# Performance work log

Measured on AMD Instinct MI355X. Metric: run time of the kernel, lower is better.

Reference implementation:

```python
import jax, jax.numpy as jnp
import numpy as np

D_MODEL = 1024
H = 16
D_K = D_MODEL // H
D_FF = 4096
EPS = 1e-6
NEG = -1e9


def layer_norm(x, alpha, beta):
    # Custom LN: scalar alpha/beta, unbiased std, eps added to std (not var)
    mean = jnp.mean(x, axis=-1, keepdims=True)
    std = jnp.std(x, axis=-1, ddof=1, keepdims=True)
    return alpha * (x - mean) / (std + EPS) + beta


def setup_inputs() -> dict:
    key = jax.random.key(0)
    ks = jax.random.split(key, 16)
    B, S = 4, 2048
    s = 1.0 / np.sqrt(D_MODEL)
    inp = {
        "x": jax.random.normal(ks[0], (B, S, D_MODEL), dtype=jnp.float32),
        "src_mask": jax.random.randint(ks[1], (B, 1, 1, S), 0, 2, dtype=jnp.int32),
        "wq": jax.random.normal(ks[2], (D_MODEL, D_MODEL), jnp.float32) * s,
        "bq": jnp.zeros((D_MODEL,), jnp.float32),
        "wk": jax.random.normal(ks[3], (D_MODEL, D_MODEL), jnp.float32) * s,
        "bk": jnp.zeros((D_MODEL,), jnp.float32),
        "wv": jax.random.normal(ks[4], (D_MODEL, D_MODEL), jnp.float32) * s,
        "bv": jnp.zeros((D_MODEL,), jnp.float32),
        "wo": jax.random.normal(ks[5], (D_MODEL, D_MODEL), jnp.float32) * s,
        "bo": jnp.zeros((D_MODEL,), jnp.float32),
        "w1": jax.random.normal(ks[6], (D_MODEL, D_FF), jnp.float32) * s,
        "b1": jnp.zeros((D_FF,), jnp.float32),
        "w2": jax.random.normal(ks[7], (D_FF, D_MODEL), jnp.float32) * (1.0 / np.sqrt(D_FF)),
        "b2": jnp.zeros((D_MODEL,), jnp.float32),
        "a1": jnp.ones((1,), jnp.float32),
        "be1": jnp.zeros((1,), jnp.float32),
        "a2": jnp.ones((1,), jnp.float32),
        "be2": jnp.zeros((1,), jnp.float32),
    }
    return inp


def reference(x, src_mask, wq, bq, wk, bk, wv, bv, wo, bo, w1, b1, w2, b2, a1, be1, a2, be2):
    B, S, _ = x.shape

    # --- residual 1: self-attention on pre-LN input (dropout = identity, eval) ---
    xn = layer_norm(x, a1, be1)
    q = (xn @ wq + bq).reshape(B, S, H, D_K).transpose(0, 2, 1, 3)  # [B,H,S,Dk]
    k = (xn @ wk + bk).reshape(B, S, H, D_K).transpose(0, 2, 1, 3)
    v = (xn @ wv + bv).reshape(B, S, H, D_K).transpose(0, 2, 1, 3)

    scores = jnp.einsum("bhqd,bhkd->bhqk", q, k) / jnp.sqrt(jnp.float32(D_K))
    scores = jnp.where(src_mask == 0, jnp.float32(NEG), scores)
    attn = jax.nn.softmax(scores, axis=-1)
    ctx = jnp.einsum("bhqk,bhkd->bhqd", attn, v)  # [B,H,S,Dk]
    ctx = ctx.transpose(0, 2, 1, 3).reshape(B, S, D_MODEL)
    attn_out = ctx @ wo + bo
    x = x + attn_out

    # --- residual 2: feed-forward on pre-LN input ---
    xn2 = layer_norm(x, a2, be2)
    ff = jax.nn.relu(xn2 @ w1 + b1) @ w2 + b2
    return x + ff
```

## Files before the change

### kernel.cpp

```cpp
#include <hip/hip_runtime.h>
#include <stdint.h>

typedef unsigned short u16;
typedef __attribute__((ext_vector_type(8))) short short8;
typedef __attribute__((ext_vector_type(4))) float f32x4;
typedef __attribute__((ext_vector_type(4))) u16 u16x4;
typedef __attribute__((ext_vector_type(4))) uint32_t u32x4;

#define NB 4
#define SEQ 2048
#define DM 1024
#define NH 16
#define DKh 64
#define DFF 4096
#define LOG2E 1.44269504089f

__device__ __forceinline__ u16 f2bf(float f) {
  union { float f; uint32_t u; } v; v.f = f;
  uint32_t u = v.u;
  return (u16)((u + 0x7FFFu + ((u >> 16) & 1u)) >> 16);
}

__device__ __forceinline__ uint32_t cvtpk(float lo, float hi) {
  uint32_t r;
  asm("v_cvt_pk_bf16_f32 %0, %1, %2" : "=v"(r) : "v"(lo), "v"(hi));
  return r;
}

__device__ __forceinline__ float fexp2(float x) {
  float r;
  asm("v_exp_f32 %0, %1" : "=v"(r) : "v"(x));
  return r;
}

__device__ __forceinline__ void gl16(const u16* g, u16* l) {
  __builtin_amdgcn_global_load_lds((const __attribute__((address_space(1))) void*)g,
                                   (__attribute__((address_space(3))) void*)l, 16, 0, 0);
}

__global__ __launch_bounds__(256) void transpose4_bf16(const float* __restrict__ s0,
                                                       const float* __restrict__ s1,
                                                       const float* __restrict__ s2,
                                                       const float* __restrict__ s3,
                                                       u16* __restrict__ d0,
                                                       u16* __restrict__ d1,
                                                       u16* __restrict__ d2,
                                                       u16* __restrict__ d3) {
  __shared__ float tile[32][33];
  int z = blockIdx.z;
  const float* src = (z == 0) ? s0 : (z == 1) ? s1 : (z == 2) ? s2 : s3;
  u16* dst = (z == 0) ? d0 : (z == 1) ? d1 : (z == 2) ? d2 : d3;
  int tx = threadIdx.x, ty = threadIdx.y;
  int c0 = blockIdx.x * 32, r0 = blockIdx.y * 32;
#pragma unroll
  for (int i = 0; i < 32; i += 8)
    tile[ty + i][tx] = src[(size_t)(r0 + ty + i) * DM + c0 + tx];
  __syncthreads();
#pragma unroll
  for (int i = 0; i < 32; i += 8)
    dst[(size_t)(c0 + ty + i) * DM + r0 + tx] = f2bf(tile[tx][ty + i]);
}

__global__ __launch_bounds__(256) void transpose_bf16(const float* __restrict__ src,
                                                      u16* __restrict__ dst, int R, int C) {
  __shared__ float tile[32][33];
  int tx = threadIdx.x, ty = threadIdx.y;
  int c0 = blockIdx.x * 32, r0 = blockIdx.y * 32;
#pragma unroll
  for (int i = 0; i < 32; i += 8)
    tile[ty + i][tx] = src[(size_t)(r0 + ty + i) * C + c0 + tx];
  __syncthreads();
#pragma unroll
  for (int i = 0; i < 32; i += 8)
    dst[(size_t)(c0 + ty + i) * R + r0 + tx] = f2bf(tile[tx][ty + i]);
}

__global__ __launch_bounds__(256) void bias_cat(const float* __restrict__ bq,
                                                const float* __restrict__ bk,
                                                const float* __restrict__ bv,
                                                float* __restrict__ o) {
  int i = blockIdx.x * 256 + threadIdx.x;
  if (i < 3072) o[i] = (i < 1024) ? bq[i] : ((i < 2048) ? bk[i - 1024] : bv[i - 2048]);
}

__global__ __launch_bounds__(1024) void compact_idx(const int* __restrict__ msk,
                                                    int* __restrict__ pinv,
                                                    int* __restrict__ lArr,
                                                    int* __restrict__ lpArr,
                                                    float* __restrict__ fbbc) {
  int b = blockIdx.x;
  int t = threadIdx.x;
  int lane = t & 63, w = t >> 6;
  int i0 = t * 2, i1 = t * 2 + 1;
  int m0 = msk[b * SEQ + i0] ? 1 : 0;
  int m1 = msk[b * SEQ + i1] ? 1 : 0;
  int s = m0 + m1;
  int run = s;
#pragma unroll
  for (int d = 1; d < 64; d <<= 1) {
    int v = __shfl_up(run, d);
    if (lane >= d) run += v;
  }
  __shared__ int wtot[16];
  __shared__ int woff[17];
  if (lane == 63) wtot[w] = run;
  __syncthreads();
  if (t == 0) {
    int acc = 0;
#pragma unroll
    for (int i = 0; i < 16; ++i) { woff[i] = acc; acc += wtot[i]; }
    woff[16] = acc;
  }
  __syncthreads();
  int excl = run - s + woff[w];
  pinv[b * SEQ + i0] = m0 ? excl : -1;
  pinv[b * SEQ + i1] = m1 ? (excl + m0) : -1;
  int L = woff[16];
  if (t == 0) {
    lArr[b] = L;
    int LP = (L + 63) & ~63;
    if (LP == 0) LP = 64;
    lpArr[b] = LP;
  }
  for (int l = t; l < SEQ; l += 1024)
    fbbc[b * SEQ + l] = (l < L) ? 0.0f : -1e9f;
}

__global__ __launch_bounds__(256) void ln_bf16(const float* __restrict__ x,
                                               u16* __restrict__ out,
                                               const float* __restrict__ alpha,
                                               const float* __restrict__ beta) {
  int row = blockIdx.x;
  const float4* xr = (const float4*)(x + (size_t)row * DM);
  int t = threadIdx.x;
  float4 v = xr[t];
  float s = v.x + v.y + v.z + v.w;
  float s2 = v.x * v.x + v.y * v.y + v.z * v.z + v.w * v.w;
#pragma unroll
  for (int m = 1; m < 64; m <<= 1) { s += __shfl_xor(s, m); s2 += __shfl_xor(s2, m); }
  __shared__ float red[8];
  int wid = t >> 6, lane = t & 63;
  if (lane == 0) { red[wid] = s; red[wid + 4] = s2; }
  __syncthreads();
  float S = red[0] + red[1] + red[2] + red[3];
  float S2 = red[4] + red[5] + red[6] + red[7];
  float mean = S * (1.0f / DM);
  float var = fmaxf((S2 - S * mean) * (1.0f / (DM - 1)), 0.0f);
  float inv = alpha[0] / (sqrtf(var) + 1e-6f);
  float bet = beta[0];
  u16x4 o;
  o[0] = f2bf((v.x - mean) * inv + bet);
  o[1] = f2bf((v.y - mean) * inv + bet);
  o[2] = f2bf((v.z - mean) * inv + bet);
  o[3] = f2bf((v.w - mean) * inv + bet);
  *(u16x4*)(out + (size_t)row * DM + t * 4) = o;
}

template <int MODE>
__global__ __launch_bounds__(512, 4) void gemm_v2(const u16* __restrict__ A,
                                                  const u16* __restrict__ WT,
                                                  const float* __restrict__ bias,
                                                  const float* __restrict__ resid,
                                                  void* __restrict__ outp,
                                                  const int* __restrict__ pinv,
                                                  int M, int N, int K, float qscale) {
  extern __shared__ u16 lds[];
  int tid = threadIdx.x;
  int lane = tid & 63, wid = tid >> 6;
  int lr = lane & 15, lg = lane >> 4;
  int wr = wid >> 1, wc = wid & 1;
  int nbx = N >> 7;
  int nwg = (M >> 8) * nbx;
  int lid = blockIdx.x;
  int swz = (lid & 7) * (nwg >> 3) + (lid >> 3);
  int m0 = (swz / nbx) << 8, n0 = (swz % nbx) << 7;

  int sr = tid >> 2;
  int sch = tid & 3;
  int scs = sch ^ ((sr >> 1) & 3);
  size_t a_src = (size_t)(m0 + sr) * K + scs * 8;
  size_t b_src = (size_t)(n0 + sr) * K + scs * 8;
  u16* a_dst = lds + sr * 32 + sch * 8;
  u16* b_dst = lds + 8192 + sr * 32 + sch * 8;

#define STAGE(B_, T_) do { \
    gl16(A + a_src + (size_t)(T_) * 32, a_dst + (B_) * 12288); \
    gl16(A + a_src + (size_t)128 * K + (size_t)(T_) * 32, a_dst + (B_) * 12288 + 4096); \
    gl16(WT + b_src + (size_t)(T_) * 32, b_dst + (B_) * 12288); \
  } while (0)

  int rchunk = (lg ^ ((lr >> 1) & 3)) * 8;
  int offA[4], offB[4];
#pragma unroll
  for (int i = 0; i < 4; ++i) offA[i] = (wr * 64 + i * 16 + lr) * 32 + rchunk;
#pragma unroll
  for (int j = 0; j < 4; ++j) offB[j] = 8192 + (wc * 64 + j * 16 + lr) * 32 + rchunk;

  f32x4 acc[4][4] = {};

  int NT = K >> 5;
  STAGE(0, 0);
  STAGE(1, 1);
  asm volatile("s_waitcnt vmcnt(3)" ::: "memory");
  __builtin_amdgcn_s_barrier();

  int buf = 0;
  for (int t = 0; t < NT; ++t) {
    const u16* la = lds + buf * 12288;
    int b2 = buf - 1; if (b2 < 0) b2 += 3;
    short8 af[4], bfr[4];
#pragma unroll
    for (int i = 0; i < 4; ++i) af[i] = *(const short8*)&la[offA[i]];
#pragma unroll
    for (int j = 0; j < 4; ++j) bfr[j] = *(const short8*)&la[offB[j]];
    if (t + 2 < NT) STAGE(b2, t + 2);
    __builtin_amdgcn_s_setprio(1);
#pragma unroll
    for (int i = 0; i < 4; ++i)
#pragma unroll
      for (int j = 0; j < 4; ++j)
        acc[i][j] = __builtin_amdgcn_mfma_f32_16x16x32_bf16(af[i], bfr[j], acc[i][j], 0, 0, 0);
    __builtin_amdgcn_s_setprio(0);
    if (t < NT - 2) asm volatile("s_waitcnt vmcnt(3)" ::: "memory");
    else            asm volatile("s_waitcnt vmcnt(0)" ::: "memory");
    __builtin_amdgcn_s_barrier();
    __builtin_amdgcn_sched_barrier(0);
    buf = (buf == 2) ? 0 : buf + 1;
  }
#undef STAGE

#pragma unroll
  for (int i = 0; i < 4; ++i) {
#pragma unroll
    for (int j = 0; j < 4; ++j) {
      int col = n0 + wc * 64 + j * 16 + lr;
      float bi = bias[col];
      int rbase = m0 + wr * 64 + i * 16 + lg * 4;
      if (MODE == 2) {
        float* o = (float*)outp;
#pragma unroll
        for (int r = 0; r < 4; ++r) {
          size_t idx = (size_t)(rbase + r) * N + col;
          o[idx] = resid[idx] + acc[i][j][r] + bi;
        }
      } else if (MODE == 3) {
        u16* o = (u16*)outp;
#pragma unroll
        for (int r = 0; r < 4; ++r)
          o[(size_t)(rbase + r) * N + col] = f2bf(fmaxf(acc[i][j][r] + bi, 0.0f));
      } else {
        u16* qb = (u16*)outp;
        int which = col >> 10, nc = col & 1023;
        int hh = nc >> 6, dd = nc & 63;
        int bb = rbase >> 11, ss = rbase & 2047;
        if (which == 0) {
#pragma unroll
          for (int r = 0; r < 4; ++r)
            qb[((size_t)(bb * NH + hh) * SEQ + (ss + r)) * DKh + dd] = f2bf((acc[i][j][r] + bi) * qscale);
        } else {
          int4 p4 = *(const int4*)(pinv + bb * SEQ + ss);
          int pos[4] = {p4.x, p4.y, p4.z, p4.w};
          if (which == 1) {
            u16* kcb = qb + (size_t)(8u << 20);
#pragma unroll
            for (int r = 0; r < 4; ++r)
              if (pos[r] >= 0)
                kcb[((size_t)(bb * NH + hh) * SEQ + pos[r]) * DKh + dd] = f2bf(acc[i][j][r] + bi);
          } else {
            u16* vcb = qb + (size_t)2 * (8u << 20);
#pragma unroll
            for (int r = 0; r < 4; ++r)
              if (pos[r] >= 0) {
                int l = pos[r];
                int lo = l & 63;
                int pi = ((lo >> 4) & 1) * 32 + ((lo >> 2) & 3) * 8 + (lo >> 5) * 4 + (lo & 3);
                vcb[((size_t)(bb * NH + hh) * DKh + dd) * SEQ + (l & ~63) + pi] = f2bf(acc[i][j][r] + bi);
              }
          }
        }
      }
    }
  }
}

__global__ __launch_bounds__(512) void attn_fwd(const u16* __restrict__ q,
                                                const u16* __restrict__ kc,
                                                const u16* __restrict__ vc,
                                                const int* __restrict__ lArr,
                                                const int* __restrict__ lpArr,
                                                const float* __restrict__ fbbc,
                                                u16* __restrict__ ctx) {
  __shared__ u16 lds[2][16384];
  int tid = threadIdx.x;
  int wid = tid >> 6, lane = tid & 63;
  int lr = lane & 15, lg = lane >> 4;
  int bh = blockIdx.x;
  int b = bh >> 4, hh = bh & 15;
  int q0 = blockIdx.y * 256 + wid * 32;
  const u16* qbase = q + (size_t)bh * SEQ * DKh;
  const u16* kcb = kc + (size_t)bh * SEQ * DKh;
  const u16* vcb = vc + (size_t)bh * DKh * SEQ;
  const float* fbbase = fbbc + b * SEQ;
  int Lb = lArr[b];
  int LP = lpArr[b];

  short8 qf[2][2];
#pragma unroll
  for (int i = 0; i < 2; ++i)
#pragma unroll
    for (int kk = 0; kk < 2; ++kk)
      qf[i][kk] = *(const short8*)(qbase + (size_t)(q0 + i * 16 + lr) * DKh + kk * 32 + lg * 8);

  int srow = tid >> 3;
  int schk = tid & 7;
  int ks0 = srow * 64 + ((schk ^ (srow & 7)) * 8);
  int vs0 = srow * SEQ + ((schk ^ (srow & 7)) * 8);
  int dst0 = tid * 8;

#define STAGE(B_, KV0) do { \
    gl16(kcb + (size_t)(KV0) * 64 + ks0, &lds[B_][dst0]); \
    gl16(kcb + (size_t)((KV0) + 64) * 64 + ks0, &lds[B_][dst0 + 4096]); \
    gl16(vcb + (size_t)(KV0) + vs0, &lds[B_][dst0 + 8192]); \
    gl16(vcb + (size_t)(KV0) + 64 + vs0, &lds[B_][dst0 + 12288]); \
  } while (0)

  int swzc = (lr & 7) << 3;

  f32x4 ot[2][4] = {};
  float mrow[2] = {-3e38f, -3e38f};
  float lsum[2] = {0.0f, 0.0f};

  STAGE(0, 0);
  asm volatile("s_waitcnt vmcnt(0)" ::: "memory");
  __builtin_amdgcn_s_barrier();

  int buf = 0;
  for (int kv0 = 0; kv0 < LP; kv0 += 128) {
    bool more = (kv0 + 128 < LP);
    if (more) STAGE(buf ^ 1, kv0 + 128);
    if (more) asm volatile("s_waitcnt vmcnt(4)" ::: "memory");
    else      asm volatile("s_waitcnt vmcnt(0)" ::: "memory");
    __builtin_amdgcn_s_barrier();

#pragma unroll
    for (int sB = 0; sB < 2; ++sB) {
      const u16* Ks = &lds[buf][sB * 4096];
      const u16* Vs = &lds[buf][8192 + sB * 4096];
      int kvs = kv0 + sB * 64;

      f32x4 st[2][4] = {};
      __builtin_amdgcn_s_setprio(1);
#pragma unroll
      for (int kk = 0; kk < 2; ++kk) {
        short8 kf[4];
#pragma unroll
        for (int j = 0; j < 4; ++j)
          kf[j] = *(const short8*)&Ks[(j * 16 + lr) * 64 + ((kk * 32 + lg * 8) ^ swzc)];
#pragma unroll
        for (int i = 0; i < 2; ++i)
#pragma unroll
          for (int j = 0; j < 4; ++j)
            st[i][j] = __builtin_amdgcn_mfma_f32_16x16x32_bf16(kf[j], qf[i][kk], st[i][j], 0, 0, 0);
      }
      __builtin_amdgcn_s_setprio(0);

      bool tail = (kvs + 64 > Lb);

      u32x4 pa[2][2];
#pragma unroll
      for (int i = 0; i < 2; ++i) {
        float p[4][4];
        if (tail) {
#pragma unroll
          for (int j = 0; j < 4; ++j) {
            float4 f4 = *(const float4*)(fbbase + kvs + j * 16 + lg * 4);
            p[j][0] = st[i][j][0] + f4.x;
            p[j][1] = st[i][j][1] + f4.y;
            p[j][2] = st[i][j][2] + f4.z;
            p[j][3] = st[i][j][3] + f4.w;
          }
        } else {
#pragma unroll
          for (int j = 0; j < 4; ++j)
#pragma unroll
            for (int r = 0; r < 4; ++r) p[j][r] = st[i][j][r];
        }
        float mx = -3e38f;
#pragma unroll
        for (int j = 0; j < 4; ++j)
#pragma unroll
          for (int r = 0; r < 4; ++r) mx = fmaxf(mx, p[j][r]);
        mx = fmaxf(mx, __shfl_xor(mx, 16));
        mx = fmaxf(mx, __shfl_xor(mx, 32));
        float mnew = fmaxf(mrow[i], mx);
        if (!__all(mnew - mrow[i] <= 8.0f)) {
          float corr = fexp2(mrow[i] - mnew);
          lsum[i] *= corr;
#pragma unroll
          for (int jd = 0; jd < 4; ++jd)
#pragma unroll
            for (int r = 0; r < 4; ++r) ot[i][jd][r] *= corr;
          mrow[i] = mnew;
        }
        float ps = 0.0f;
#pragma unroll
        for (int j = 0; j < 4; ++j)
#pragma unroll
          for (int r = 0; r < 4; ++r) {
            float pv = fexp2(p[j][r] - mrow[i]);
            p[j][r] = pv;
            ps += pv;
          }
        ps += __shfl_xor(ps, 16);
        ps += __shfl_xor(ps, 32);
        lsum[i] += ps;
#pragma unroll
        for (int ks = 0; ks < 2; ++ks) {
          pa[i][ks][0] = cvtpk(p[ks][0], p[ks][1]);
          pa[i][ks][1] = cvtpk(p[ks][2], p[ks][3]);
          pa[i][ks][2] = cvtpk(p[ks + 2][0], p[ks + 2][1]);
          pa[i][ks][3] = cvtpk(p[ks + 2][2], p[ks + 2][3]);
        }
      }

      __builtin_amdgcn_s_setprio(1);
#pragma unroll
      for (int ks = 0; ks < 2; ++ks) {
        short8 vf[4];
#pragma unroll
        for (int jd = 0; jd < 4; ++jd)
          vf[jd] = *(const short8*)&Vs[(jd * 16 + lr) * 64 + ((ks * 32 + lg * 8) ^ swzc)];
#pragma unroll
        for (int i = 0; i < 2; ++i)
#pragma unroll
          for (int jd = 0; jd < 4; ++jd)
            ot[i][jd] = __builtin_amdgcn_mfma_f32_16x16x32_bf16(vf[jd], *(short8*)&pa[i][ks], ot[i][jd], 0, 0, 0);
      }
      __builtin_amdgcn_s_setprio(0);
    }
    __builtin_amdgcn_s_barrier();
    buf ^= 1;
  }
#undef STAGE

  asm volatile("s_waitcnt vmcnt(0)" ::: "memory");
  __builtin_amdgcn_s_barrier();

  float inv0 = 1.0f / lsum[0], inv1 = 1.0f / lsum[1];
  u16* ep = &lds[0][wid * 2048];
#pragma unroll
  for (int i = 0; i < 2; ++i) {
    float inv = i ? inv1 : inv0;
#pragma unroll
    for (int jd = 0; jd < 4; ++jd) {
      uint32_t w0 = cvtpk(ot[i][jd][0] * inv, ot[i][jd][1] * inv);
      uint32_t w1 = cvtpk(ot[i][jd][2] * inv, ot[i][jd][3] * inv);
      uint32_t pk2[2] = {w0, w1};
      *(u16x4*)&ep[(i * 16 + lr) * 64 + ((jd * 16 + lg * 4) ^ swzc)] = *(u16x4*)pk2;
    }
  }
  __syncthreads();
  int q_ = lane >> 1;
  size_t orow = ((size_t)b * SEQ + q0 + q_) * DM + hh * DKh;
#pragma unroll
  for (int it = 0; it < 4; ++it) {
    int dc = (lane & 1) * 32 + it * 8;
    short8 vv = *(const short8*)&ep[q_ * 64 + (dc ^ ((q_ & 7) << 3))];
    *(short8*)(ctx + orow + dc) = vv;
  }
}

extern "C" void kernel_launch(void* const* d_in, const int* in_sizes, int n_in,
                              void* d_out, int out_size, void* d_ws, size_t ws_size,
                              hipStream_t stream) {
  const float* x   = (const float*)d_in[0];
  const int*   msk = (const int*)d_in[1];
  const float* wq  = (const float*)d_in[2];
  const float* bq  = (const float*)d_in[3];
  const float* wk  = (const float*)d_in[4];
  const float* bk  = (const float*)d_in[5];
  const float* wv  = (const float*)d_in[6];
  const float* bv  = (const float*)d_in[7];
  const float* wo  = (const float*)d_in[8];
  const float* bo  = (const float*)d_in[9];
  const float* w1  = (const float*)d_in[10];
  const float* b1  = (const float*)d_in[11];
  const float* w2  = (const float*)d_in[12];
  const float* b2  = (const float*)d_in[13];
  const float* a1  = (const float*)d_in[14];
  const float* be1 = (const float*)d_in[15];
  const float* a2  = (const float*)d_in[16];
  const float* be2 = (const float*)d_in[17];
  float* out = (float*)d_out;

  u16* wqT = (u16*)d_ws;
  u16* wkT = wqT + (1u << 20);
  u16* wvT = wkT + (1u << 20);
  u16* woT = wvT + (1u << 20);
  u16* w1T = woT + (1u << 20);
  u16* w2T = w1T + (4u << 20);
  u16* xn  = w2T + (4u << 20);
  u16* qb  = xn  + (8u << 20);
  u16* kb  = qb  + (8u << 20);
  u16* vtb = kb  + (8u << 20);
  u16* ctx = vtb + (8u << 20);
  u16* hb  = qb;
  float* bcat = (float*)ctx;
  int*   pinv = (int*)(ctx + (8u << 20));
  int*   lArr = pinv + NB * SEQ;
  int*   lpArr = lArr + 16;
  float* fbbc = (float*)(lpArr + 16);

  (void)hipFuncSetAttribute((const void*)gemm_v2<0>, hipFuncAttributeMaxDynamicSharedMemorySize, 72 * 1024);
  (void)hipFuncSetAttribute((const void*)gemm_v2<2>, hipFuncAttributeMaxDynamicSharedMemorySize, 72 * 1024);
  (void)hipFuncSetAttribute((const void*)gemm_v2<3>, hipFuncAttributeMaxDynamicSharedMemorySize, 72 * 1024);

  dim3 tb(32, 8);
  transpose4_bf16<<<dim3(32, 32, 4), tb, 0, stream>>>(wq, wk, wv, wo, wqT, wkT, wvT, woT);
  transpose_bf16<<<dim3(128, 32), tb, 0, stream>>>(w1, w1T, DM, DFF);
  transpose_bf16<<<dim3(32, 128), tb, 0, stream>>>(w2, w2T, DFF, DM);
  bias_cat<<<12, 256, 0, stream>>>(bq, bk, bv, bcat);
  compact_idx<<<NB, 1024, 0, stream>>>(msk, pinv, lArr, lpArr, fbbc);

  ln_bf16<<<NB * SEQ, 256, 0, stream>>>(x, xn, a1, be1);

  gemm_v2<0><<<768, 512, 72 * 1024, stream>>>(xn, wqT, bcat, nullptr, qb, pinv, NB * SEQ, 3 * DM, DM, 0.125f * LOG2E);

  attn_fwd<<<dim3(NB * NH, SEQ / 256), 512, 0, stream>>>(qb, kb, vtb, lArr, lpArr, fbbc, ctx);

  gemm_v2<2><<<256, 512, 72 * 1024, stream>>>(ctx, woT, bo, x, out, nullptr, NB * SEQ, DM, DM, 1.0f);

  ln_bf16<<<NB * SEQ, 256, 0, stream>>>(out, xn, a2, be2);

  gemm_v2<3><<<1024, 512, 72 * 1024, stream>>>(xn, w1T, b1, nullptr, hb, nullptr, NB * SEQ, DFF, DM, 1.0f);

  gemm_v2<2><<<256, 512, 72 * 1024, stream>>>(hb, w2T, b2, out, out, nullptr, NB * SEQ, DM, DFF, 1.0f);
}
```

Measured before the change: 349.3 us.

## Double GEMM K-tile to 64 with 8-chunk XOR swizzle and merge prep kernels

The GEMM now stages a 64-wide K slice per pipeline step instead of 32. It uses six 16-byte global-to-LDS loads per thread and a new 8-way XOR swizzle, and issues two MFMA k-substeps per barrier. This halves the number of loop iterations and barriers per GEMM. In exchange, LDS use doubles to 144 KB for three buffers and launch bounds drop to 2 blocks per SM, which reduces occupancy. The separate weight-transpose and bias-concat kernels are also merged into one prep launch to cut launch overhead.

```diff
diff --git a/kernel.cpp b/kernel.cpp
--- a/kernel.cpp
+++ b/kernel.cpp
@@ -38,34 +38,34 @@
                                    (__attribute__((address_space(3))) void*)l, 16, 0, 0);
 }
 
-__global__ __launch_bounds__(256) void transpose4_bf16(const float* __restrict__ s0,
-                                                       const float* __restrict__ s1,
-                                                       const float* __restrict__ s2,
-                                                       const float* __restrict__ s3,
-                                                       u16* __restrict__ d0,
-                                                       u16* __restrict__ d1,
-                                                       u16* __restrict__ d2,
-                                                       u16* __restrict__ d3) {
+__global__ __launch_bounds__(256) void prep(const float* __restrict__ wq, const float* __restrict__ wk,
+                                            const float* __restrict__ wv, const float* __restrict__ wo,
+                                            const float* __restrict__ w1, const float* __restrict__ w2,
+                                            u16* __restrict__ wqT, u16* __restrict__ wkT,
+                                            u16* __restrict__ wvT, u16* __restrict__ woT,
+                                            u16* __restrict__ w1T, u16* __restrict__ w2T,
+                                            const float* __restrict__ bq, const float* __restrict__ bk,
+                                            const float* __restrict__ bv, float* __restrict__ bcat) {
+  int idx = blockIdx.x;
+  int tx = threadIdx.x, ty = threadIdx.y;
+  if (idx >= 12288) {
+    int i = (idx - 12288) * 256 + ty * 32 + tx;
+    if (i < 3072) bcat[i] = (i < 1024) ? bq[i] : ((i < 2048) ? bk[i - 1024] : bv[i - 2048]);
+    return;
+  }
+  const float* src; u16* dst; int R, C, bx, by;
+  if (idx < 4096) {
+    int z = idx >> 10;
+    src = (z == 0) ? wq : (z == 1) ? wk : (z == 2) ? wv : wo;
+    dst = (z == 0) ? wqT : (z == 1) ? wkT : (z == 2) ? wvT : woT;
+    R = DM; C = DM; int i = idx & 1023; bx = i & 31; by = i >> 5;
+  } else if (idx < 8192) {
+    src = w1; dst = w1T; R = DM; C = DFF; int i = idx - 4096; bx = i & 127; by = i >> 7;
+  } else {
+    src = w2; dst = w2T; R = DFF; C = DM; int i = idx - 8192; bx = i & 31; by = i >> 5;
+  }
   __shared__ float tile[32][33];
-  int z = blockIdx.z;
-  const float* src = (z == 0) ? s0 : (z == 1) ? s1 : (z == 2) ? s2 : s3;
-  u16* dst = (z == 0) ? d0 : (z == 1) ? d1 : (z == 2) ? d2 : d3;
-  int tx = threadIdx.x, ty = threadIdx.y;
-  int c0 = blockIdx.x * 32, r0 = blockIdx.y * 32;
-#pragma unroll
-  for (int i = 0; i < 32; i += 8)
-    tile[ty + i][tx] = src[(size_t)(r0 + ty + i) * DM + c0 + tx];
-  __syncthreads();
-#pragma unroll
-  for (int i = 0; i < 32; i += 8)
-    dst[(size_t)(c0 + ty + i) * DM + r0 + tx] = f2bf(tile[tx][ty + i]);
-}
-
-__global__ __launch_bounds__(256) void transpose_bf16(const float* __restrict__ src,
-                                                      u16* __restrict__ dst, int R, int C) {
-  __shared__ float tile[32][33];
-  int tx = threadIdx.x, ty = threadIdx.y;
-  int c0 = blockIdx.x * 32, r0 = blockIdx.y * 32;
+  int c0 = bx * 32, r0 = by * 32;
 #pragma unroll
   for (int i = 0; i < 32; i += 8)
     tile[ty + i][tx] = src[(size_t)(r0 + ty + i) * C + c0 + tx];
@@ -73,14 +73,6 @@
 #pragma unroll
   for (int i = 0; i < 32; i += 8)
     dst[(size_t)(c0 + ty + i) * R + r0 + tx] = f2bf(tile[tx][ty + i]);
-}
-
-__global__ __launch_bounds__(256) void bias_cat(const float* __restrict__ bq,
-                                                const float* __restrict__ bk,
-                                                const float* __restrict__ bv,
-                                                float* __restrict__ o) {
-  int i = blockIdx.x * 256 + threadIdx.x;
-  if (i < 3072) o[i] = (i < 1024) ? bq[i] : ((i < 2048) ? bk[i - 1024] : bv[i - 2048]);
 }
 
 __global__ __launch_bounds__(1024) void compact_idx(const int* __restrict__ msk,
@@ -157,7 +149,7 @@
 }
 
 template <int MODE>
-__global__ __launch_bounds__(512, 4) void gemm_v2(const u16* __restrict__ A,
+__global__ __launch_bounds__(512, 2) void gemm_v2(const u16* __restrict__ A,
                                                   const u16* __restrict__ WT,
                                                   const float* __restrict__ bias,
                                                   const float* __restrict__ resid,
@@ -175,53 +167,66 @@
   int swz = (lid & 7) * (nwg >> 3) + (lid >> 3);
   int m0 = (swz / nbx) << 8, n0 = (swz % nbx) << 7;
 
-  int sr = tid >> 2;
-  int sch = tid & 3;
-  int scs = sch ^ ((sr >> 1) & 3);
-  size_t a_src = (size_t)(m0 + sr) * K + scs * 8;
-  size_t b_src = (size_t)(n0 + sr) * K + scs * 8;
-  u16* a_dst = lds + sr * 32 + sch * 8;
-  u16* b_dst = lds + 8192 + sr * 32 + sch * 8;
+  int sr2 = tid >> 3;
+  int sch2 = tid & 7;
+  int csrc8 = (sch2 ^ (sr2 & 7)) * 8;
+  size_t a_src = (size_t)(m0 + sr2) * K + csrc8;
+  size_t b_src = (size_t)(n0 + sr2) * K + csrc8;
+  u16* dstb = lds + tid * 8;
 
 #define STAGE(B_, T_) do { \
-    gl16(A + a_src + (size_t)(T_) * 32, a_dst + (B_) * 12288); \
-    gl16(A + a_src + (size_t)128 * K + (size_t)(T_) * 32, a_dst + (B_) * 12288 + 4096); \
-    gl16(WT + b_src + (size_t)(T_) * 32, b_dst + (B_) * 12288); \
+    const u16* as_ = A + a_src + (size_t)(T_) * 64; \
+    gl16(as_,                   dstb + (B_) * 24576); \
+    gl16(as_ + (size_t)64 * K,  dstb + (B_) * 24576 + 4096); \
+    gl16(as_ + (size_t)128 * K, dstb + (B_) * 24576 + 8192); \
+    gl16(as_ + (size_t)192 * K, dstb + (B_) * 24576 + 12288); \
+    const u16* bs_ = WT + b_src + (size_t)(T_) * 64; \
+    gl16(bs_,                   dstb + (B_) * 24576 + 16384); \
+    gl16(bs_ + (size_t)64 * K,  dstb + (B_) * 24576 + 20480); \
   } while (0)
 
-  int rchunk = (lg ^ ((lr >> 1) & 3)) * 8;
+  int xo8 = lr & 7;
+  int ckk[2] = {((0 + lg) ^ xo8) * 8, ((4 + lg) ^ xo8) * 8};
   int offA[4], offB[4];
 #pragma unroll
-  for (int i = 0; i < 4; ++i) offA[i] = (wr * 64 + i * 16 + lr) * 32 + rchunk;
-#pragma unroll
-  for (int j = 0; j < 4; ++j) offB[j] = 8192 + (wc * 64 + j * 16 + lr) * 32 + rchunk;
+  for (int i = 0; i < 4; ++i) offA[i] = (wr * 64 + i * 16 + lr) * 64;
+#pragma unroll
+  for (int j = 0; j < 4; ++j) offB[j] = 16384 + (wc * 64 + j * 16 + lr) * 64;
 
   f32x4 acc[4][4] = {};
 
-  int NT = K >> 5;
+  int NT = K >> 6;
   STAGE(0, 0);
   STAGE(1, 1);
-  asm volatile("s_waitcnt vmcnt(3)" ::: "memory");
+  asm volatile("s_waitcnt vmcnt(6)" ::: "memory");
   __builtin_amdgcn_s_barrier();
 
   int buf = 0;
   for (int t = 0; t < NT; ++t) {
-    const u16* la = lds + buf * 12288;
+    const u16* la = lds + buf * 24576;
     int b2 = buf - 1; if (b2 < 0) b2 += 3;
-    short8 af[4], bfr[4];
-#pragma unroll
-    for (int i = 0; i < 4; ++i) af[i] = *(const short8*)&la[offA[i]];
-#pragma unroll
-    for (int j = 0; j < 4; ++j) bfr[j] = *(const short8*)&la[offB[j]];
+    short8 af[4][2], bfr[4][2];
+#pragma unroll
+    for (int i = 0; i < 4; ++i) {
+      af[i][0] = *(const short8*)&la[offA[i] + ckk[0]];
+      af[i][1] = *(const short8*)&la[offA[i] + ckk[1]];
+    }
+#pragma unroll
+    for (int j = 0; j < 4; ++j) {
+      bfr[j][0] = *(const short8*)&la[offB[j] + ckk[0]];
+      bfr[j][1] = *(const short8*)&la[offB[j] + ckk[1]];
+    }
     if (t + 2 < NT) STAGE(b2, t + 2);
     __builtin_amdgcn_s_setprio(1);
 #pragma unroll
-    for (int i = 0; i < 4; ++i)
-#pragma unroll
-      for (int j = 0; j < 4; ++j)
-        acc[i][j] = __builtin_amdgcn_mfma_f32_16x16x32_bf16(af[i], bfr[j], acc[i][j], 0, 0, 0);
+    for (int kk = 0; kk < 2; ++kk)
+#pragma unroll
+      for (int i = 0; i < 4; ++i)
+#pragma unroll
+        for (int j = 0; j < 4; ++j)
+          acc[i][j] = __builtin_amdgcn_mfma_f32_16x16x32_bf16(af[i][kk], bfr[j][kk], acc[i][j], 0, 0, 0);
     __builtin_amdgcn_s_setprio(0);
-    if (t < NT - 2) asm volatile("s_waitcnt vmcnt(3)" ::: "memory");
+    if (t < NT - 2) asm volatile("s_waitcnt vmcnt(6)" ::: "memory");
     else            asm volatile("s_waitcnt vmcnt(0)" ::: "memory");
     __builtin_amdgcn_s_barrier();
     __builtin_amdgcn_sched_barrier(0);
@@ -511,28 +516,25 @@
   int*   lpArr = lArr + 16;
   float* fbbc = (float*)(lpArr + 16);
 
-  (void)hipFuncSetAttribute((const void*)gemm_v2<0>, hipFuncAttributeMaxDynamicSharedMemorySize, 72 * 1024);
-  (void)hipFuncSetAttribute((const void*)gemm_v2<2>, hipFuncAttributeMaxDynamicSharedMemorySize, 72 * 1024);
-  (void)hipFuncSetAttribute((const void*)gemm_v2<3>, hipFuncAttributeMaxDynamicSharedMemorySize, 72 * 1024);
+  (void)hipFuncSetAttribute((const void*)gemm_v2<0>, hipFuncAttributeMaxDynamicSharedMemorySize, 144 * 1024);
+  (void)hipFuncSetAttribute((const void*)gemm_v2<2>, hipFuncAttributeMaxDynamicSharedMemorySize, 144 * 1024);
+  (void)hipFuncSetAttribute((const void*)gemm_v2<3>, hipFuncAttributeMaxDynamicSharedMemorySize, 144 * 1024);
 
   dim3 tb(32, 8);
-  transpose4_bf16<<<dim3(32, 32, 4), tb, 0, stream>>>(wq, wk, wv, wo, wqT, wkT, wvT, woT);
-  transpose_bf16<<<dim3(128, 32), tb, 0, stream>>>(w1, w1T, DM, DFF);
-  transpose_bf16<<<dim3(32, 128), tb, 0, stream>>>(w2, w2T, DFF, DM);
-  bias_cat<<<12, 256, 0, stream>>>(bq, bk, bv, bcat);
+  prep<<<12300, tb, 0, stream>>>(wq, wk, wv, wo, w1, w2, wqT, wkT, wvT, woT, w1T, w2T, bq, bk, bv, bcat);
   compact_idx<<<NB, 1024, 0, stream>>>(msk, pinv, lArr, lpArr, fbbc);
 
   ln_bf16<<<NB * SEQ, 256, 0, stream>>>(x, xn, a1, be1);
 
-  gemm_v2<0><<<768, 512, 72 * 1024, stream>>>(xn, wqT, bcat, nullptr, qb, pinv, NB * SEQ, 3 * DM, DM, 0.125f * LOG2E);
+  gemm_v2<0><<<768, 512, 144 * 1024, stream>>>(xn, wqT, bcat, nullptr, qb, pinv, NB * SEQ, 3 * DM, DM, 0.125f * LOG2E);
 
   attn_fwd<<<dim3(NB * NH, SEQ / 256), 512, 0, stream>>>(qb, kb, vtb, lArr, lpArr, fbbc, ctx);
 
-  gemm_v2<2><<<256, 512, 72 * 1024, stream>>>(ctx, woT, bo, x, out, nullptr, NB * SEQ, DM, DM, 1.0f);
+  gemm_v2<2><<<256, 512, 144 * 1024, stream>>>(ctx, woT, bo, x, out, nullptr, NB * SEQ, DM, DM, 1.0f);
 
   ln_bf16<<<NB * SEQ, 256, 0, stream>>>(out, xn, a2, be2);
 
-  gemm_v2<3><<<1024, 512, 72 * 1024, stream>>>(xn, w1T, b1, nullptr, hb, nullptr, NB * SEQ, DFF, DM, 1.0f);
-
-  gemm_v2<2><<<256, 512, 72 * 1024, stream>>>(hb, w2T, b2, out, out, nullptr, NB * SEQ, DM, DFF, 1.0f);
-}
+  gemm_v2<3><<<1024, 512, 144 * 1024, stream>>>(xn, w1T, b1, nullptr, hb, nullptr, NB * SEQ, DFF, DM, 1.0f);
+
+  gemm_v2<2><<<256, 512, 144 * 1024, stream>>>(hb, w2T, b2, out, out, nullptr, NB * SEQ, DM, DFF, 1.0f);
+}
```

Result: slower. 358.5 us (+2.6%).
